# Kernel tuning notes

Measured on AMD Instinct MI355X. Metric: run time of the kernel, lower is better.

## Reference

```python
import jax, jax.numpy as jnp
import numpy as np

I, H, C = 256, 512, 1024
TY, TX, B = 32, 128, 32


def setup_inputs() -> dict:
    key = jax.random.key(0)
    ks = jax.random.split(key, 16)
    s = lambda k, shape: jax.random.normal(k, shape, dtype=jnp.float32) * 0.05
    return {
        "y_emb": jax.random.normal(ks[0], (TY, B, I), dtype=jnp.float32),
        "context": jax.random.normal(ks[1], (TX, B, C), dtype=jnp.float32),
        "init_h": jax.random.normal(ks[2], (B, H), dtype=jnp.float32),
        "init_c": jax.random.normal(ks[3], (B, H), dtype=jnp.float32),
        "x_mask": jnp.ones((TX, B, 1), dtype=jnp.float32),
        "y_mask": jnp.ones((TY, B, 1), dtype=jnp.float32),
        "W": s(ks[4], (4 * H, I)),
        "U": s(ks[5], (4 * H, H)),
        "b": jnp.zeros((4 * H,), dtype=jnp.float32),
        "Wx": s(ks[6], (4 * H, C)),
        "Ux": s(ks[7], (4 * H, H)),
        "bx": jnp.zeros((4 * H,), dtype=jnp.float32),
        "Wc_att": s(ks[8], (C, C)),
        "b_att": jnp.zeros((C,), dtype=jnp.float32),
        "W_comb_att": s(ks[9], (C, H)),
        "U_att": s(ks[10], (1, C)),
    }


def _decode(y_emb, context, init_h, init_c, x_mask, y_mask,
            W, U, b, Wx, Ux, bx, Wc_att, b_att, W_comb_att, U_att):
    pctx = jnp.einsum('tbc,dc->tbd', context, Wc_att) + b_att  # [Tx,B,C]
    x = jnp.einsum('tbi,gi->tbg', y_emb, W) + b                # [Ty,B,4H]

    def step(carry, inp):
        pre_h, pre_c = carry
        xt, ymt = inp  # [B,4H], [B,1]
        pre1 = xt + pre_h @ U.T
        i1, f1, o1, g1 = jnp.split(pre1, 4, axis=1)
        c1 = jax.nn.sigmoid(f1) * pre_c + jax.nn.sigmoid(i1) * jnp.tanh(g1)
        h1 = jax.nn.sigmoid(o1) * jnp.tanh(c1)
        h1 = ymt * h1 + (1.0 - ymt) * pre_h
        # Bahdanau attention over source positions (dim 0)
        hproj = h1 @ W_comb_att.T                      # [B,C]
        unreg = jnp.tanh(pctx + hproj) * x_mask        # [Tx,B,C]
        score = unreg @ U_att.T                        # [Tx,B,1]
        att = jnp.exp(score - jnp.max(score, axis=0, keepdims=True)) * x_mask
        att = att / jnp.sum(att, axis=0, keepdims=True)
        atted = jnp.sum(att * context, axis=0)         # [B,C]
        pre2 = h1 @ Ux.T + atted @ Wx.T + bx
        i2, f2, o2, g2 = jnp.split(pre2, 4, axis=1)
        c2 = jax.nn.sigmoid(f2) * c1 + jax.nn.sigmoid(i2) * jnp.tanh(g2)
        h2 = jax.nn.sigmoid(o2) * jnp.tanh(c2)
        h2 = ymt * h2 + (1.0 - ymt) * h1
        return (h2, c2), (h2, c2, atted)

    _, (hs, cs, atts) = jax.lax.scan(step, (init_h, init_c), (x, y_mask))
    return hs, cs, atts


def reference(y_emb, context, init_h, init_c, x_mask, y_mask,
              W, U, b, Wx, Ux, bx, Wc_att, b_att, W_comb_att, U_att):
    hs, cs, atts = _decode(y_emb, context, init_h, init_c, x_mask, y_mask,
                           W, U, b, Wx, Ux, bx, Wc_att, b_att, W_comb_att, U_att)
    return ((hs, cs), atts)
```

## Files before the change

### kernel.cpp

```cpp
#include <hip/hip_runtime.h>

#define DEV static __device__ __forceinline__

DEV float sigf(float x) { return 1.0f / (1.0f + __expf(-x)); }
DEV float ftanh(float x) {
  float xc = fminf(fmaxf(x, -9.0f), 9.0f);
  float e = __expf(2.0f * xc);
  return (e - 1.0f) / (e + 1.0f);
}

__global__ __launch_bounds__(256) void gemm_nt_bias(
    const float* __restrict__ A, const float* __restrict__ B,
    const float* __restrict__ bias, float* __restrict__ out,
    int M, int N, int K)
{
  __shared__ float As[64][17];
  __shared__ float Bs[64][17];
  const int tid = threadIdx.x;
  const int m0 = blockIdx.y * 64, n0 = blockIdx.x * 64;
  const int lr = tid >> 2;
  const int lk = (tid & 3) << 2;
  const int ty = tid >> 4, tx = tid & 15;
  float acc[4][4] = {};
  for (int k0 = 0; k0 < K; k0 += 16) {
    float4 a4 = *(const float4*)(A + (size_t)(m0 + lr) * K + k0 + lk);
    float4 b4 = *(const float4*)(B + (size_t)(n0 + lr) * K + k0 + lk);
    As[lr][lk] = a4.x; As[lr][lk + 1] = a4.y; As[lr][lk + 2] = a4.z; As[lr][lk + 3] = a4.w;
    Bs[lr][lk] = b4.x; Bs[lr][lk + 1] = b4.y; Bs[lr][lk + 2] = b4.z; Bs[lr][lk + 3] = b4.w;
    __syncthreads();
#pragma unroll
    for (int kk = 0; kk < 16; ++kk) {
      float av[4], bv[4];
#pragma unroll
      for (int r = 0; r < 4; ++r) av[r] = As[ty * 4 + r][kk];
#pragma unroll
      for (int c = 0; c < 4; ++c) bv[c] = Bs[tx * 4 + c][kk];
#pragma unroll
      for (int r = 0; r < 4; ++r)
#pragma unroll
        for (int c = 0; c < 4; ++c) acc[r][c] = fmaf(av[r], bv[c], acc[r][c]);
    }
    __syncthreads();
  }
#pragma unroll
  for (int r = 0; r < 4; ++r) {
    int m = m0 + ty * 4 + r;
#pragma unroll
    for (int c = 0; c < 4; ++c) {
      int n = n0 + tx * 4 + c;
      out[(size_t)m * N + n] = acc[r][c] + bias[n];
    }
  }
}

__global__ void transpose_h(const float* __restrict__ src ,
                            float* __restrict__ dstT )
{
  int idx = blockIdx.x * 256 + threadIdx.x;
  if (idx < 4096) {
    int k4 = idx >> 5, b = idx & 31;
    ((float4*)dstT)[idx] = ((const float4*)src)[b * 128 + k4];
  }
}

__global__ __launch_bounds__(256) void lstm1_k(
    const float* __restrict__ xt, const float* __restrict__ hT,
    const float* __restrict__ cprev, const float* __restrict__ U,
    const float* __restrict__ ym,
    float* __restrict__ h1, float* __restrict__ h1T, float* __restrict__ c1)
{
  const int tid = threadIdx.x;
  const int b = tid & 31;
  const int slot = tid >> 5;
  const int kh = slot & 1;
  const int gate = slot >> 1;
  const int j = blockIdx.x;
  const float* urow = U + (size_t)(gate * 512 + j) * 512 + kh * 256;
  const float4* h4p = (const float4*)hT + kh * 64 * 32;
  float acc = 0.f;
#pragma unroll 8
  for (int k4 = 0; k4 < 64; ++k4) {
    float4 h4 = h4p[k4 * 32 + b];
    float4 u4 = *(const float4*)(urow + k4 * 4);
    acc = fmaf(h4.x, u4.x, fmaf(h4.y, u4.y, fmaf(h4.z, u4.z, fmaf(h4.w, u4.w, acc))));
  }
  __shared__ float lds[256];
  lds[slot * 32 + b] = acc;
  __syncthreads();
  if (tid < 32) {
    const int b2 = tid;
    float pi = xt[b2 * 2048 + j]        + lds[b2]        + lds[32 + b2];
    float pf = xt[b2 * 2048 + 512 + j]  + lds[64 + b2]   + lds[96 + b2];
    float po = xt[b2 * 2048 + 1024 + j] + lds[128 + b2]  + lds[160 + b2];
    float pg = xt[b2 * 2048 + 1536 + j] + lds[192 + b2]  + lds[224 + b2];
    float cold = cprev[b2 * 512 + j];
    float cn = sigf(pf) * cold + sigf(pi) * tanhf(pg);
    float hn = sigf(po) * tanhf(cn);
    float ymv = ym[b2];
    float hfall = hT[(j >> 2) * 128 + b2 * 4 + (j & 3)];
    float hm = ymv * hn + (1.f - ymv) * hfall;
    h1[b2 * 512 + j] = hm;
    h1T[(j >> 2) * 128 + b2 * 4 + (j & 3)] = hm;
    c1[b2 * 512 + j] = cn;
  }
}

__global__ __launch_bounds__(256) void hproj_k(
    const float* __restrict__ h1T, const float* __restrict__ Wcomb,
    float* __restrict__ hproj)
{
  const int tid = threadIdx.x;
  const int b = tid & 31;
  const int dl = (tid >> 5) & 1;
  const int kq = tid >> 6;
  const int d = blockIdx.x * 2 + dl;
  const float* wrow = Wcomb + (size_t)d * 512 + kq * 128;
  const float4* h4p = (const float4*)h1T + kq * 32 * 32;
  float acc = 0.f;
#pragma unroll 8
  for (int k4 = 0; k4 < 32; ++k4) {
    float4 h4 = h4p[k4 * 32 + b];
    float4 w4 = *(const float4*)(wrow + k4 * 4);
    acc = fmaf(h4.x, w4.x, fmaf(h4.y, w4.y, fmaf(h4.z, w4.z, fmaf(h4.w, w4.w, acc))));
  }
  __shared__ float lds[256];
  lds[tid] = acc;
  __syncthreads();
  if (tid < 64) {
    const int bb = tid & 31, dll = tid >> 5;
    float s = lds[dll * 32 + bb] + lds[64 + dll * 32 + bb]
            + lds[128 + dll * 32 + bb] + lds[192 + dll * 32 + bb];
    hproj[bb * 1024 + blockIdx.x * 2 + dll] = s;
  }
}

__global__ __launch_bounds__(256) void score_k(
    const float* __restrict__ pctx, const float* __restrict__ hproj,
    const float* __restrict__ U_att, const float* __restrict__ x_mask,
    float* __restrict__ evals )
{
  const int t = blockIdx.x;
  const int b = blockIdx.y * 4 + (threadIdx.x >> 6);
  const int lane = threadIdx.x & 63;
  const float4* pr = (const float4*)(pctx + ((size_t)t * 32 + b) * 1024);
  const float4* hp = (const float4*)(hproj + (size_t)b * 1024);
  const float4* ua = (const float4*)U_att;
  float acc = 0.f;
#pragma unroll
  for (int i = 0; i < 4; ++i) {
    int c4 = i * 64 + lane;
    float4 p = pr[c4], h = hp[c4], u = ua[c4];
    acc += ftanh(p.x + h.x) * u.x + ftanh(p.y + h.y) * u.y
         + ftanh(p.z + h.z) * u.z + ftanh(p.w + h.w) * u.w;
  }
#pragma unroll
  for (int off = 32; off > 0; off >>= 1) acc += __shfl_down(acc, off);
  if (lane == 0) {
    float xm = x_mask[t * 32 + b];
    evals[t * 32 + b] = __expf(acc * xm) * xm;
  }
}

__global__ __launch_bounds__(256) void atted_k(
    const float* __restrict__ evals, const float* __restrict__ context,
    float* __restrict__ atts_t , float* __restrict__ attedT)
{
  const int b = blockIdx.x, cc = blockIdx.y;
  const int tid = threadIdx.x;
  __shared__ float sc[128];
  __shared__ float red;
  __shared__ float4 part[8][32];
  if (tid < 128) sc[tid] = evals[tid * 32 + b];
  __syncthreads();
  if (tid < 64) {
    float s = sc[tid] + sc[tid + 64];
#pragma unroll
    for (int off = 32; off > 0; off >>= 1) s += __shfl_down(s, off);
    if (tid == 0) red = s;
  }
  __syncthreads();
  const float inv = 1.0f / red;
  const int c4 = tid & 31, tg = tid >> 5;
  const float4* ctx4 = (const float4*)context;
  float4 acc = make_float4(0.f, 0.f, 0.f, 0.f);
  for (int t = tg; t < 128; t += 8) {
    float a = sc[t];
    float4 v = ctx4[((size_t)t * 32 + b) * 256 + cc * 32 + c4];
    acc.x = fmaf(a, v.x, acc.x); acc.y = fmaf(a, v.y, acc.y);
    acc.z = fmaf(a, v.z, acc.z); acc.w = fmaf(a, v.w, acc.w);
  }
  part[tg][c4] = acc;
  __syncthreads();
  if (tid < 32) {
    float4 tot = part[0][tid];
#pragma unroll
    for (int g = 1; g < 8; ++g) {
      float4 p = part[g][tid];
      tot.x += p.x; tot.y += p.y; tot.z += p.z; tot.w += p.w;
    }
    tot.x *= inv; tot.y *= inv; tot.z *= inv; tot.w *= inv;
    ((float4*)(atts_t + (size_t)b * 1024 + cc * 128))[tid] = tot;
    const int cbase = cc * 32 + tid;
    ((float4*)attedT)[(size_t)cbase * 32 + b] = tot;
  }
}

__global__ __launch_bounds__(256) void lstm2_k(
    const float* __restrict__ h1, const float* __restrict__ h1T,
    const float* __restrict__ c1, const float* __restrict__ attT,
    const float* __restrict__ Ux, const float* __restrict__ Wx,
    const float* __restrict__ bx, const float* __restrict__ ym,
    float* __restrict__ hs_t, float* __restrict__ cs_t,
    float* __restrict__ hT_next)
{
  const int tid = threadIdx.x;
  const int b = tid & 31;
  const int slot = tid >> 5;
  const int kh = slot & 1;
  const int gate = slot >> 1;
  const int j = blockIdx.x;
  const float* uxrow = Ux + (size_t)(gate * 512 + j) * 512 + kh * 256;
  const float* wxrow = Wx + (size_t)(gate * 512 + j) * 1024 + kh * 512;
  const float4* h4p = (const float4*)h1T + kh * 64 * 32;
  const float4* a4p = (const float4*)attT + kh * 128 * 32;
  float acc = 0.f;
#pragma unroll 8
  for (int k4 = 0; k4 < 64; ++k4) {
    float4 h4 = h4p[k4 * 32 + b];
    float4 u4 = *(const float4*)(uxrow + k4 * 4);
    acc = fmaf(h4.x, u4.x, fmaf(h4.y, u4.y, fmaf(h4.z, u4.z, fmaf(h4.w, u4.w, acc))));
  }
#pragma unroll 8
  for (int c4 = 0; c4 < 128; ++c4) {
    float4 v4 = a4p[c4 * 32 + b];
    float4 w4 = *(const float4*)(wxrow + c4 * 4);
    acc = fmaf(v4.x, w4.x, fmaf(v4.y, w4.y, fmaf(v4.z, w4.z, fmaf(v4.w, w4.w, acc))));
  }
  __shared__ float lds[256];
  lds[slot * 32 + b] = acc;
  __syncthreads();
  if (tid < 32) {
    const int b2 = tid;
    float pi = bx[j]        + lds[b2]       + lds[32 + b2];
    float pf = bx[512 + j]  + lds[64 + b2]  + lds[96 + b2];
    float po = bx[1024 + j] + lds[128 + b2] + lds[160 + b2];
    float pg = bx[1536 + j] + lds[192 + b2] + lds[224 + b2];
    float c1v = c1[b2 * 512 + j];
    float cn = sigf(pf) * c1v + sigf(pi) * tanhf(pg);
    float hn = sigf(po) * tanhf(cn);
    float ymv = ym[b2];
    float hf = h1[b2 * 512 + j];
    float hm = ymv * hn + (1.f - ymv) * hf;
    hs_t[b2 * 512 + j] = hm;
    cs_t[b2 * 512 + j] = cn;
    hT_next[(j >> 2) * 128 + b2 * 4 + (j & 3)] = hm;
  }
}

extern "C" void kernel_launch(void* const* d_in, const int* in_sizes, int n_in,
                              void* d_out, int out_size, void* d_ws, size_t ws_size,
                              hipStream_t stream)
{
  const float* y_emb   = (const float*)d_in[0];
  const float* context = (const float*)d_in[1];
  const float* init_h  = (const float*)d_in[2];
  const float* init_c  = (const float*)d_in[3];
  const float* x_mask  = (const float*)d_in[4];
  const float* y_mask  = (const float*)d_in[5];
  const float* W       = (const float*)d_in[6];
  const float* U       = (const float*)d_in[7];
  const float* bvec    = (const float*)d_in[8];
  const float* Wx      = (const float*)d_in[9];
  const float* Ux      = (const float*)d_in[10];
  const float* bx      = (const float*)d_in[11];
  const float* Wc      = (const float*)d_in[12];
  const float* b_att   = (const float*)d_in[13];
  const float* Wcomb   = (const float*)d_in[14];
  const float* U_att   = (const float*)d_in[15];

  float* out  = (float*)d_out;
  float* hs   = out;
  float* cs   = out + (size_t)32 * 32 * 512;
  float* atts = out + (size_t)2 * 32 * 32 * 512;

  float* ws    = (float*)d_ws;
  float* pctx  = ws;
  float* x     = pctx + 4194304;
  float* h1    = x + 2097152;
  float* c1    = h1 + 16384;
  float* hproj = c1 + 16384;
  float* evals = hproj + 32768;
  float* hT    = evals + 4096;
  float* h1T   = hT + 16384;
  float* attT  = h1T + 16384;

  gemm_nt_bias<<<dim3(16, 64), 256, 0, stream>>>(context, Wc, b_att, pctx, 4096, 1024, 1024);
  gemm_nt_bias<<<dim3(32, 16), 256, 0, stream>>>(y_emb, W, bvec, x, 1024, 2048, 256);
  transpose_h<<<16, 256, 0, stream>>>(init_h, hT);

  for (int t = 0; t < 32; ++t) {
    const float* cp = t ? cs + (size_t)(t - 1) * 16384 : init_c;
    lstm1_k<<<512, 256, 0, stream>>>(x + (size_t)t * 65536, hT, cp, U, y_mask + t * 32, h1, h1T, c1);
    hproj_k<<<512, 256, 0, stream>>>(h1T, Wcomb, hproj);
    score_k<<<dim3(128, 8), 256, 0, stream>>>(pctx, hproj, U_att, x_mask, evals);
    atted_k<<<dim3(32, 8), 256, 0, stream>>>(evals, context, atts + (size_t)t * 32768, attT);
    lstm2_k<<<512, 256, 0, stream>>>(h1, h1T, c1, attT, Ux, Wx, bx, y_mask + t * 32,
                                     hs + (size_t)t * 16384, cs + (size_t)t * 16384, hT);
  }
}
```

Before: 2.039 ms.

## Fuse attention projection, scoring and context sum into one per-batch kernel

Replaces the separate hproj, score and atted kernels with a single attn_k launched with one 1024-thread block per batch element. Intermediates (hproj, scores, normaliser) stay in shared memory, which removes two launches per step and the global round trips between them. The trade-off is only 32 blocks, so the work uses a small fraction of the GPU's compute units. Each block also re-reads all of Wcomb (2 MB) and streams its batch slice of pctx and context.

```diff
diff --git a/kernel.cpp b/kernel.cpp
--- a/kernel.cpp
+++ b/kernel.cpp
@@ -105,103 +105,105 @@
   }
 }
 
-__global__ __launch_bounds__(256) void hproj_k(
-    const float* __restrict__ h1T, const float* __restrict__ Wcomb,
-    float* __restrict__ hproj)
-{
+__global__ __launch_bounds__(1024) void attn_k(
+    const float* __restrict__ h1,
+    const float* __restrict__ Wcomb,
+    const float* __restrict__ U_att,
+    const float* __restrict__ x_mask,
+    const float* __restrict__ pctx,
+    const float* __restrict__ context,
+    float* __restrict__ atts_t,
+    float* __restrict__ attT)
+{
+  const int b = blockIdx.x;
   const int tid = threadIdx.x;
-  const int b = tid & 31;
-  const int dl = (tid >> 5) & 1;
-  const int kq = tid >> 6;
-  const int d = blockIdx.x * 2 + dl;
-  const float* wrow = Wcomb + (size_t)d * 512 + kq * 128;
-  const float4* h4p = (const float4*)h1T + kq * 32 * 32;
-  float acc = 0.f;
-#pragma unroll 8
-  for (int k4 = 0; k4 < 32; ++k4) {
-    float4 h4 = h4p[k4 * 32 + b];
-    float4 w4 = *(const float4*)(wrow + k4 * 4);
-    acc = fmaf(h4.x, w4.x, fmaf(h4.y, w4.y, fmaf(h4.z, w4.z, fmaf(h4.w, w4.w, acc))));
-  }
-  __shared__ float lds[256];
-  lds[tid] = acc;
+  __shared__ float hsh[512];
+  __shared__ float hp[1024];
+  __shared__ float ev[128];
+  __shared__ float invs;
+  __shared__ float4 part[4][256];
+
+  if (tid < 512) hsh[tid] = h1[b * 512 + tid];
+  __syncthreads();
+
+  {
+    const int wv = tid >> 6;
+    const int lane = tid & 63;
+    const int hl = lane >> 5;
+    const int kl = lane & 31;
+    const float4* hs4 = (const float4*)hsh;
+    float4 h0 = hs4[kl], h1r = hs4[kl + 32], h2r = hs4[kl + 64], h3r = hs4[kl + 96];
+    const float4* w4 = (const float4*)Wcomb;
+#pragma unroll 4
+    for (int i = 0; i < 32; ++i) {
+      int c = wv * 64 + i * 2 + hl;
+      const float4* wr = w4 + (size_t)c * 128;
+      float4 w0 = wr[kl], w1 = wr[kl + 32], w2 = wr[kl + 64], w3 = wr[kl + 96];
+      float acc = h0.x * w0.x + h0.y * w0.y + h0.z * w0.z + h0.w * w0.w;
+      acc = fmaf(h1r.x, w1.x, fmaf(h1r.y, w1.y, fmaf(h1r.z, w1.z, fmaf(h1r.w, w1.w, acc))));
+      acc = fmaf(h2r.x, w2.x, fmaf(h2r.y, w2.y, fmaf(h2r.z, w2.z, fmaf(h2r.w, w2.w, acc))));
+      acc = fmaf(h3r.x, w3.x, fmaf(h3r.y, w3.y, fmaf(h3r.z, w3.z, fmaf(h3r.w, w3.w, acc))));
+#pragma unroll
+      for (int off = 16; off > 0; off >>= 1) acc += __shfl_down(acc, off, 32);
+      if (kl == 0) hp[c] = acc;
+    }
+  }
+  __syncthreads();
+
+  {
+    const int t = tid >> 3, cc = tid & 7;
+    const float4* pr = (const float4*)(pctx + ((size_t)t * 32 + b) * 1024) + cc * 32;
+    const float4* hpp = (const float4*)hp + cc * 32;
+    const float4* ua = (const float4*)U_att + cc * 32;
+    float acc = 0.f;
+#pragma unroll 8
+    for (int i = 0; i < 32; ++i) {
+      float4 pv = pr[i], hv = hpp[i], uv = ua[i];
+      acc += ftanh(pv.x + hv.x) * uv.x + ftanh(pv.y + hv.y) * uv.y
+           + ftanh(pv.z + hv.z) * uv.z + ftanh(pv.w + hv.w) * uv.w;
+    }
+    acc += __shfl_down(acc, 4, 8);
+    acc += __shfl_down(acc, 2, 8);
+    acc += __shfl_down(acc, 1, 8);
+    if (cc == 0) {
+      float xm = x_mask[t * 32 + b];
+      ev[t] = __expf(acc * xm) * xm;
+    }
+  }
   __syncthreads();
   if (tid < 64) {
-    const int bb = tid & 31, dll = tid >> 5;
-    float s = lds[dll * 32 + bb] + lds[64 + dll * 32 + bb]
-            + lds[128 + dll * 32 + bb] + lds[192 + dll * 32 + bb];
-    hproj[bb * 1024 + blockIdx.x * 2 + dll] = s;
-  }
-}
-
-__global__ __launch_bounds__(256) void score_k(
-    const float* __restrict__ pctx, const float* __restrict__ hproj,
-    const float* __restrict__ U_att, const float* __restrict__ x_mask,
-    float* __restrict__ evals )
-{
-  const int t = blockIdx.x;
-  const int b = blockIdx.y * 4 + (threadIdx.x >> 6);
-  const int lane = threadIdx.x & 63;
-  const float4* pr = (const float4*)(pctx + ((size_t)t * 32 + b) * 1024);
-  const float4* hp = (const float4*)(hproj + (size_t)b * 1024);
-  const float4* ua = (const float4*)U_att;
-  float acc = 0.f;
-#pragma unroll
-  for (int i = 0; i < 4; ++i) {
-    int c4 = i * 64 + lane;
-    float4 p = pr[c4], h = hp[c4], u = ua[c4];
-    acc += ftanh(p.x + h.x) * u.x + ftanh(p.y + h.y) * u.y
-         + ftanh(p.z + h.z) * u.z + ftanh(p.w + h.w) * u.w;
-  }
-#pragma unroll
-  for (int off = 32; off > 0; off >>= 1) acc += __shfl_down(acc, off);
-  if (lane == 0) {
-    float xm = x_mask[t * 32 + b];
-    evals[t * 32 + b] = __expf(acc * xm) * xm;
-  }
-}
-
-__global__ __launch_bounds__(256) void atted_k(
-    const float* __restrict__ evals, const float* __restrict__ context,
-    float* __restrict__ atts_t , float* __restrict__ attedT)
-{
-  const int b = blockIdx.x, cc = blockIdx.y;
-  const int tid = threadIdx.x;
-  __shared__ float sc[128];
-  __shared__ float red;
-  __shared__ float4 part[8][32];
-  if (tid < 128) sc[tid] = evals[tid * 32 + b];
-  __syncthreads();
-  if (tid < 64) {
-    float s = sc[tid] + sc[tid + 64];
+    float s = ev[tid] + ev[tid + 64];
 #pragma unroll
     for (int off = 32; off > 0; off >>= 1) s += __shfl_down(s, off);
-    if (tid == 0) red = s;
-  }
-  __syncthreads();
-  const float inv = 1.0f / red;
-  const int c4 = tid & 31, tg = tid >> 5;
-  const float4* ctx4 = (const float4*)context;
-  float4 acc = make_float4(0.f, 0.f, 0.f, 0.f);
-  for (int t = tg; t < 128; t += 8) {
-    float a = sc[t];
-    float4 v = ctx4[((size_t)t * 32 + b) * 256 + cc * 32 + c4];
-    acc.x = fmaf(a, v.x, acc.x); acc.y = fmaf(a, v.y, acc.y);
-    acc.z = fmaf(a, v.z, acc.z); acc.w = fmaf(a, v.w, acc.w);
-  }
-  part[tg][c4] = acc;
-  __syncthreads();
-  if (tid < 32) {
-    float4 tot = part[0][tid];
-#pragma unroll
-    for (int g = 1; g < 8; ++g) {
-      float4 p = part[g][tid];
-      tot.x += p.x; tot.y += p.y; tot.z += p.z; tot.w += p.w;
-    }
-    tot.x *= inv; tot.y *= inv; tot.z *= inv; tot.w *= inv;
-    ((float4*)(atts_t + (size_t)b * 1024 + cc * 128))[tid] = tot;
-    const int cbase = cc * 32 + tid;
-    ((float4*)attedT)[(size_t)cbase * 32 + b] = tot;
+    if (tid == 0) invs = 1.0f / s;
+  }
+  __syncthreads();
+
+  {
+    const int c4 = tid & 255, tq = tid >> 8;
+    const float4* ctx4 = (const float4*)context;
+    float4 acc = make_float4(0.f, 0.f, 0.f, 0.f);
+#pragma unroll 8
+    for (int i = 0; i < 32; ++i) {
+      int t = tq * 32 + i;
+      float a = ev[t];
+      float4 v = ctx4[((size_t)t * 32 + b) * 256 + c4];
+      acc.x = fmaf(a, v.x, acc.x); acc.y = fmaf(a, v.y, acc.y);
+      acc.z = fmaf(a, v.z, acc.z); acc.w = fmaf(a, v.w, acc.w);
+    }
+    part[tq][c4] = acc;
+  }
+  __syncthreads();
+  if (tid < 256) {
+    float4 p0 = part[0][tid], p1 = part[1][tid], p2 = part[2][tid], p3 = part[3][tid];
+    float4 tot;
+    const float inv = invs;
+    tot.x = (p0.x + p1.x + p2.x + p3.x) * inv;
+    tot.y = (p0.y + p1.y + p2.y + p3.y) * inv;
+    tot.z = (p0.z + p1.z + p2.z + p3.z) * inv;
+    tot.w = (p0.w + p1.w + p2.w + p3.w) * inv;
+    ((float4*)(atts_t + (size_t)b * 1024))[tid] = tot;
+    ((float4*)attT)[(size_t)tid * 32 + b] = tot;
   }
 }
 
@@ -288,9 +290,7 @@
   float* x     = pctx + 4194304;
   float* h1    = x + 2097152;
   float* c1    = h1 + 16384;
-  float* hproj = c1 + 16384;
-  float* evals = hproj + 32768;
-  float* hT    = evals + 4096;
+  float* hT    = c1 + 16384;
   float* h1T   = hT + 16384;
   float* attT  = h1T + 16384;
 
@@ -301,9 +301,8 @@
   for (int t = 0; t < 32; ++t) {
     const float* cp = t ? cs + (size_t)(t - 1) * 16384 : init_c;
     lstm1_k<<<512, 256, 0, stream>>>(x + (size_t)t * 65536, hT, cp, U, y_mask + t * 32, h1, h1T, c1);
-    hproj_k<<<512, 256, 0, stream>>>(h1T, Wcomb, hproj);
-    score_k<<<dim3(128, 8), 256, 0, stream>>>(pctx, hproj, U_att, x_mask, evals);
-    atted_k<<<dim3(32, 8), 256, 0, stream>>>(evals, context, atts + (size_t)t * 32768, attT);
+    attn_k<<<32, 1024, 0, stream>>>(h1, Wcomb, U_att, x_mask, pctx, context,
+                                    atts + (size_t)t * 32768, attT);
     lstm2_k<<<512, 256, 0, stream>>>(h1, h1T, c1, attT, Ux, Wx, bx, y_mask + t * 32,
                                      hs + (size_t)t * 16384, cs + (size_t)t * 16384, hT);
   }
```

Result: slower. 3.177 ms (+55.8%).
